# Performance work log

Hardware: AMD Instinct MI355X
Metric: run time of the kernel (lower is better)

The kernel has to match this reference:

```python
import jax, jax.numpy as jnp
import numpy as np

N, E = 50000, 800000
IN_C, HID, OUT_C = 100, 128, 40
LAYERS, GROUPS, CODES = 3, 3, 16
BETA = 0.98
EPS = 1e-5


def setup_inputs() -> dict:
    key = jax.random.key(0)
    ks = jax.random.split(key, 16)
    lin = lambda k, i, o: (jax.random.normal(k, (i, o), jnp.float32) / np.sqrt(i)).astype(jnp.float32)
    d = {}
    d["x"] = jax.random.normal(ks[0], (N, IN_C), jnp.float32)
    d["src"] = jax.random.randint(ks[1], (E,), 0, N, jnp.int32)
    d["dst"] = jax.random.randint(ks[2], (E,), 0, N, jnp.int32)
    # SAGEConv params: lin_l (aggregated, with bias) and lin_r (root, no bias)
    d["W0a"], d["W0r"], d["b0"] = lin(ks[3], IN_C, HID), lin(ks[4], IN_C, HID), jnp.zeros((HID,), jnp.float32)
    d["W1a"], d["W1r"], d["b1"] = lin(ks[5], HID, HID), lin(ks[6], HID, HID), jnp.zeros((HID,), jnp.float32)
    d["W2a"], d["W2r"], d["b2"] = lin(ks[7], HID, HID), lin(ks[8], HID, HID), jnp.zeros((HID,), jnp.float32)
    # BatchNorm (eval mode: running stats) for first num_layers-1 = 2 layers
    d["bn_gamma"] = jnp.ones((2, HID), jnp.float32)
    d["bn_beta"] = jnp.zeros((2, HID), jnp.float32)
    d["bn_mean"] = jnp.zeros((2, HID), jnp.float32)
    d["bn_var"] = jnp.ones((2, HID), jnp.float32)
    # Residual VQ codebooks: [layer, group, num_codes, feature]
    d["codebooks"] = 0.1 * jax.random.normal(ks[9], (LAYERS, GROUPS, CODES, HID), jnp.float32)
    d["lin_W"] = lin(ks[10], HID, OUT_C)
    d["lin_b"] = jnp.zeros((OUT_C,), jnp.float32)
    return d


def _sage_conv(h, src, dst, Wa, Wr, b):
    # mean neighbor aggregation (PyG SAGEConv, aggr='mean')
    msg = h[src]                                              # [E, d]
    agg = jax.ops.segment_sum(msg, dst, num_segments=N)       # [N, d]
    deg = jax.ops.segment_sum(jnp.ones((E,), h.dtype), dst, num_segments=N)
    agg = agg / jnp.maximum(deg, 1.0)[:, None]
    return agg @ Wa + b + h @ Wr


def _rvq(h, cb):
    # residual vector quantization over GROUPS codebooks; cb: [G, K, D]
    res, quant, ids = h, jnp.zeros_like(h), []
    for g in range(GROUPS):
        c = cb[g]                                             # [K, D]
        d2 = (jnp.sum(res * res, -1, keepdims=True)
              - 2.0 * res @ c.T + jnp.sum(c * c, -1))          # [N, K]
        idx = jnp.argmin(d2, axis=-1)
        q = c[idx]
        quant = quant + q
        res = res - q
        ids.append(idx)
    sg = jax.lax.stop_gradient
    loss = (BETA * jnp.mean((h - sg(quant)) ** 2)
            + (1.0 - BETA) * jnp.mean((sg(h) - quant) ** 2))
    return loss, jnp.stack(ids, axis=1)                        # [N, G] int


def reference(x, src, dst, W0a, W0r, b0, W1a, W1r, b1, W2a, W2r, b2,
              bn_gamma, bn_beta, bn_mean, bn_var, codebooks, lin_W, lin_b):
    Ws = [(W0a, W0r, b0), (W1a, W1r, b1), (W2a, W2r, b2)]
    h = x
    total_loss = jnp.float32(0.0)
    id_list = []
    for i in range(LAYERS - 1):
        h = _sage_conv(h, src, dst, *Ws[i])
        h = (h - bn_mean[i]) * jax.lax.rsqrt(bn_var[i] + EPS) * bn_gamma[i] + bn_beta[i]
        h = jax.nn.relu(h)                                     # dropout: eval mode (identity)
        loss, ids = _rvq(h, codebooks[i])
        total_loss = total_loss + loss
        id_list.append(ids)
    h = _sage_conv(h, src, dst, *Ws[-1])
    loss, ids = _rvq(h, codebooks[-1])
    total_loss = total_loss + loss
    id_list.append(ids)
    out = h @ lin_W + lin_b
    return out, total_loss, jnp.concatenate(id_list, axis=1)
```

## Files before the change

### kernel.cpp

```cpp
#include <hip/hip_runtime.h>

#define NN 50000
#define HID 128
#define IN_C 100
#define OUT_C 40

__global__ __launch_bounds__(256)
void hist_kernel(const int* __restrict__ dst, int* __restrict__ deg, int E) {
    int e = blockIdx.x * 256 + threadIdx.x;
    if (e < E) atomicAdd(&deg[dst[e]], 1);
}

__global__ __launch_bounds__(256)
void chunk_sum_kernel(const int* __restrict__ deg, int* __restrict__ chunk_sums, int N) {
    __shared__ int s[256];
    const int t = threadIdx.x;
    const int i = blockIdx.x * 256 + t;
    s[t] = (i < N) ? deg[i] : 0;
    __syncthreads();
    for (int o = 128; o; o >>= 1) { if (t < o) s[t] += s[t + o]; __syncthreads(); }
    if (t == 0) chunk_sums[blockIdx.x] = s[0];
}

__global__ __launch_bounds__(256)
void chunk_scan_kernel(int* __restrict__ chunk_sums, int M) {
    __shared__ int s[256];
    const int t = threadIdx.x;
    int v = (t < M) ? chunk_sums[t] : 0;
    s[t] = v;
    __syncthreads();
    for (int o = 1; o < 256; o <<= 1) {
        int x = (t >= o) ? s[t - o] : 0;
        __syncthreads();
        s[t] += x;
        __syncthreads();
    }
    if (t < M) chunk_sums[t] = s[t] - v;
}

__global__ __launch_bounds__(256)
void chunk_apply_kernel(const int* __restrict__ deg, const int* __restrict__ chunk_sums,
                        int* __restrict__ row_start, int* __restrict__ cursor, int N) {
    __shared__ int s[256];
    const int t = threadIdx.x;
    const int i = blockIdx.x * 256 + t;
    int v = (i < N) ? deg[i] : 0;
    s[t] = v;
    __syncthreads();
    for (int o = 1; o < 256; o <<= 1) {
        int x = (t >= o) ? s[t - o] : 0;
        __syncthreads();
        s[t] += x;
        __syncthreads();
    }
    if (i < N) {
        int ex = chunk_sums[blockIdx.x] + s[t] - v;
        row_start[i] = ex;
        cursor[i] = ex;
        if (i == N - 1) row_start[N] = ex + v;
    }
}

__global__ __launch_bounds__(256)
void scatter_kernel(const int* __restrict__ src, const int* __restrict__ dst,
                    int* __restrict__ cursor, int* __restrict__ csr_src, int E) {
    int e = blockIdx.x * 256 + threadIdx.x;
    if (e < E) {
        int pos = atomicAdd(&cursor[dst[e]], 1);
        csr_src[pos] = src[e];
    }
}

template<int K, bool HAS_BN, typename TIN>
__global__ __launch_bounds__(512, 6)
void layer_fused(const TIN* __restrict__ h_in,
                 const int* __restrict__ row_start, const int* __restrict__ csr_src,
                 const float* __restrict__ Wa, const float* __restrict__ Wr,
                 const float* __restrict__ b,
                 const float* __restrict__ gamma, const float* __restrict__ beta,
                 const float* __restrict__ mean, const float* __restrict__ var,
                 const float* __restrict__ cb,
                 double* __restrict__ h_out,
                 float* __restrict__ ids_out, int id_col0,
                 double* __restrict__ loss_part) {
    __shared__ double s_agg[8][HID];
    __shared__ double s_h[8][HID];
    __shared__ float s_cb[3 * 16 * 129];
    __shared__ float s_cc32[3][16];
    __shared__ double s_ws[8];
    const int t = threadIdx.x;
    const int w = t >> 6, lane = t & 63;
    const int n0 = blockIdx.x * 8;

    {
        const int n = n0 + w;
        const int r0 = row_start[n], r1 = row_start[n + 1];
        const int f0 = 2 * lane;
        if (f0 < K) {
            double a0 = 0.0, a1 = 0.0, c0 = 0.0, c1 = 0.0;
            int i = r0;
            for (; i + 1 < r1; i += 2) {
                const TIN* p0 = h_in + (size_t)csr_src[i] * K + f0;
                const TIN* p1 = h_in + (size_t)csr_src[i + 1] * K + f0;
                a0 += (double)p0[0]; a1 += (double)p0[1];
                c0 += (double)p1[0]; c1 += (double)p1[1];
            }
            if (i < r1) {
                const TIN* p0 = h_in + (size_t)csr_src[i] * K + f0;
                a0 += (double)p0[0]; a1 += (double)p0[1];
            }
            const int deg = r1 - r0;
            const double dd = (double)(deg > 1 ? deg : 1);
            const TIN* pr = h_in + (size_t)n * K + f0;
            s_agg[w][f0]     = (a0 + c0) / dd;
            s_agg[w][f0 + 1] = (a1 + c1) / dd;
            s_h[w][f0]     = (double)pr[0];
            s_h[w][f0 + 1] = (double)pr[1];
        }
    }
    __syncthreads();

    for (int idx = t; idx < 3 * 16 * 128; idx += 512)
        s_cb[(idx >> 7) * 129 + (idx & 127)] = cb[idx];

    const int col = t & 127;
    const int p4 = t >> 7;
    double accA = (double)b[col];
    double accB = accA;
#pragma unroll 4
    for (int k = 0; k < K; ++k) {
        const double wa = (double)Wa[(size_t)k * HID + col];
        const double wr = (double)Wr[(size_t)k * HID + col];
        accA += s_agg[p4][k] * wa + s_h[p4][k] * wr;
        accB += s_agg[p4 + 4][k] * wa + s_h[p4 + 4][k] * wr;
    }
    __syncthreads();

    {
        double scale = 1.0, shift = 0.0;
        if (HAS_BN) {
            scale = (double)gamma[col] / sqrt((double)var[col] + 1e-5);
            shift = (double)beta[col] - (double)mean[col] * scale;
        }
        double vA = accA, vB = accB;
        if (HAS_BN) {
            vA = vA * scale + shift; vA = vA > 0.0 ? vA : 0.0;
            vB = vB * scale + shift; vB = vB > 0.0 ? vB : 0.0;
        }
        h_out[(size_t)(n0 + p4) * HID + col] = vA;
        h_out[(size_t)(n0 + p4 + 4) * HID + col] = vB;
        s_agg[p4][col] = vA;
        s_agg[p4 + 4][col] = vB;
    }
    if (t < 48) {
        const float* c = &s_cb[t * 129];
        double s = 0.0;
        for (int j = 0; j < 128; j++) { double cj = (double)c[j]; s += cj * cj; }
        s_cc32[t >> 4][t & 15] = (float)s;
    }
    __syncthreads();

    {
        double* res = &s_agg[w][0];
        const int n = n0 + w;
        const int k = lane & 15, q = lane >> 4;

        for (int g = 0; g < 3; ++g) {
            double r0 = res[lane], r1 = res[lane + 64];
            double pr = r0 * r0 + r1 * r1;
            pr += __shfl_xor(pr, 1, 64);
            pr += __shfl_xor(pr, 2, 64);
            pr += __shfl_xor(pr, 4, 64);
            pr += __shfl_xor(pr, 8, 64);
            pr += __shfl_xor(pr, 16, 64);
            pr += __shfl_xor(pr, 32, 64);
            const float rr32 = (float)pr;

            const float* c = &s_cb[(g * 16 + k) * 129];
            double dot = 0.0;
#pragma unroll
            for (int j2 = 0; j2 < 32; ++j2) {
                int j = q * 32 + ((j2 + q * 8) & 31);
                dot += res[j] * (double)c[j];
            }
            dot += __shfl_xor(dot, 16, 64);
            dot += __shfl_xor(dot, 32, 64);

            const float rc32 = (float)dot;
            const float t1 = rr32 - 2.0f * rc32;
            const float d2 = t1 + s_cc32[g][k];

            float bv = d2; int bk = k;
            {
                float ov; int ok;
                ov = __shfl_xor(bv, 1, 64); ok = __shfl_xor(bk, 1, 64);
                if (ov < bv || (ov == bv && ok < bk)) { bv = ov; bk = ok; }
                ov = __shfl_xor(bv, 2, 64); ok = __shfl_xor(bk, 2, 64);
                if (ov < bv || (ov == bv && ok < bk)) { bv = ov; bk = ok; }
                ov = __shfl_xor(bv, 4, 64); ok = __shfl_xor(bk, 4, 64);
                if (ov < bv || (ov == bv && ok < bk)) { bv = ov; bk = ok; }
                ov = __shfl_xor(bv, 8, 64); ok = __shfl_xor(bk, 8, 64);
                if (ov < bv || (ov == bv && ok < bk)) { bv = ov; bk = ok; }
            }
            if (lane == 0)
                ids_out[(size_t)n * 9 + id_col0 + g] = (float)bk;

            res[lane]      -= (double)s_cb[(g * 16 + bk) * 129 + lane];
            res[lane + 64] -= (double)s_cb[(g * 16 + bk) * 129 + lane + 64];
        }
        double r0 = res[lane], r1 = res[lane + 64];
        double wl = r0 * r0 + r1 * r1;
        wl += __shfl_xor(wl, 1, 64);
        wl += __shfl_xor(wl, 2, 64);
        wl += __shfl_xor(wl, 4, 64);
        wl += __shfl_xor(wl, 8, 64);
        wl += __shfl_xor(wl, 16, 64);
        wl += __shfl_xor(wl, 32, 64);
        if (lane == 0) s_ws[w] = wl;
    }
    __syncthreads();
    if (t == 0) {
        double s = 0.0;
#pragma unroll
        for (int i = 0; i < 8; i++) s += s_ws[i];
        loss_part[blockIdx.x] = s;
    }
}

__global__ __launch_bounds__(128)
void linear_kernel(const double* __restrict__ h, const float* __restrict__ W,
                   const float* __restrict__ b, float* __restrict__ out, int N) {
    constexpr int NODES = 32;
    __shared__ float s_w[HID * OUT_C];
    __shared__ float s_b[OUT_C];
    __shared__ double s_h[HID];
    const int t = threadIdx.x;
    for (int idx = t; idx < HID * OUT_C; idx += 128) s_w[idx] = W[idx];
    if (t < OUT_C) s_b[t] = b[t];
    __syncthreads();
    const int n0 = blockIdx.x * NODES;
    for (int ni = 0; ni < NODES; ++ni) {
        int n = n0 + ni;
        if (n >= N) break;
        s_h[t] = h[(size_t)n * HID + t];
        __syncthreads();
        if (t < OUT_C) {
            double acc = (double)s_b[t];
            for (int kk = 0; kk < HID; kk++)
                acc += s_h[kk] * (double)s_w[kk * OUT_C + t];
            out[(size_t)n * OUT_C + t] = (float)acc;
        }
        __syncthreads();
    }
}

__global__ __launch_bounds__(256)
void finalize_kernel(const double* __restrict__ loss_part, int M,
                     float* __restrict__ out_loss) {
    __shared__ double s[256];
    const int t = threadIdx.x;
    double v = 0.0;
    for (int i = t; i < M; i += 256) v += loss_part[i];
    s[t] = v;
    __syncthreads();
    for (int off = 128; off; off >>= 1) {
        if (t < off) s[t] += s[t + off];
        __syncthreads();
    }
    if (t == 0) out_loss[0] = (float)(s[0] / ((double)NN * (double)HID));
}

extern "C" void kernel_launch(void* const* d_in, const int* in_sizes, int n_in,
                              void* d_out, int out_size, void* d_ws, size_t ws_size,
                              hipStream_t stream) {
    const float* x    = (const float*)d_in[0];
    const int*   src  = (const int*)d_in[1];
    const int*   dst  = (const int*)d_in[2];
    const float* W0a = (const float*)d_in[3];
    const float* W0r = (const float*)d_in[4];
    const float* b0  = (const float*)d_in[5];
    const float* W1a = (const float*)d_in[6];
    const float* W1r = (const float*)d_in[7];
    const float* b1  = (const float*)d_in[8];
    const float* W2a = (const float*)d_in[9];
    const float* W2r = (const float*)d_in[10];
    const float* b2  = (const float*)d_in[11];
    const float* bn_gamma = (const float*)d_in[12];
    const float* bn_beta  = (const float*)d_in[13];
    const float* bn_mean  = (const float*)d_in[14];
    const float* bn_var   = (const float*)d_in[15];
    const float* cb    = (const float*)d_in[16];
    const float* lin_W = (const float*)d_in[17];
    const float* lin_b = (const float*)d_in[18];

    const int E = in_sizes[1];

    float* out      = (float*)d_out;
    float* out_loss = out + (size_t)NN * OUT_C;
    float* out_ids  = out_loss + 1;

    char* base = (char*)d_ws;
    int* deg_i      = (int*)base;
    int* row_start  = deg_i + NN;
    int* cursor     = row_start + NN + 1;
    int* csr_src    = cursor + NN;
    int* chunk_sums = csr_src + E;
    size_t int_bytes = ((size_t)(3 * NN + 1 + E + 256) * 4 + 255) & ~(size_t)255;
    double* loss_part = (double*)(base + int_bytes);
    double* h1 = loss_part + 3 * 6250 + 6;
    double* h2 = h1 + (size_t)NN * HID;

    const int cb_layer = 3 * 16 * HID;
    const int NB = NN / 8;
    const int NCHUNK = (NN + 255) / 256;

    hipMemsetAsync(deg_i, 0, NN * sizeof(int), stream);
    hist_kernel<<<(E + 255) / 256, 256, 0, stream>>>(dst, deg_i, E);
    chunk_sum_kernel<<<NCHUNK, 256, 0, stream>>>(deg_i, chunk_sums, NN);
    chunk_scan_kernel<<<1, 256, 0, stream>>>(chunk_sums, NCHUNK);
    chunk_apply_kernel<<<NCHUNK, 256, 0, stream>>>(deg_i, chunk_sums, row_start, cursor, NN);
    scatter_kernel<<<(E + 255) / 256, 256, 0, stream>>>(src, dst, cursor, csr_src, E);

    layer_fused<IN_C, true, float><<<NB, 512, 0, stream>>>(
        x, row_start, csr_src, W0a, W0r, b0, bn_gamma, bn_beta, bn_mean, bn_var,
        cb + 0 * cb_layer, h1, out_ids, 0, loss_part);

    layer_fused<HID, true, double><<<NB, 512, 0, stream>>>(
        h1, row_start, csr_src, W1a, W1r, b1,
        bn_gamma + HID, bn_beta + HID, bn_mean + HID, bn_var + HID,
        cb + 1 * cb_layer, h2, out_ids, 3, loss_part + NB);

    layer_fused<HID, false, double><<<NB, 512, 0, stream>>>(
        h2, row_start, csr_src, W2a, W2r, b2, nullptr, nullptr, nullptr, nullptr,
        cb + 2 * cb_layer, h1, out_ids, 6, loss_part + 2 * NB);

    linear_kernel<<<(NN + 31) / 32, 128, 0, stream>>>(h1, lin_W, lin_b, out, NN);
    finalize_kernel<<<1, 256, 0, stream>>>(loss_part, 3 * NB, out_loss);
}
```

Measured before the change: 1.029 ms.

## Fold BatchNorm into pre-converted double2 weights and vectorize gather and GEMV

```diff
diff --git a/kernel.cpp b/kernel.cpp
--- a/kernel.cpp
+++ b/kernel.cpp
@@ -71,101 +71,128 @@
     }
 }
 
-template<int K, bool HAS_BN, typename TIN>
-__global__ __launch_bounds__(512, 6)
+__global__ __launch_bounds__(128)
+void prep_weights(const float* __restrict__ Wa, const float* __restrict__ Wr,
+                  const float* __restrict__ b,
+                  const float* __restrict__ gamma, const float* __restrict__ beta,
+                  const float* __restrict__ mean, const float* __restrict__ var,
+                  int has_bn,
+                  double2* __restrict__ Wa2, double2* __restrict__ Wr2,
+                  double* __restrict__ b64) {
+    const int col = threadIdx.x;
+    const int k2 = blockIdx.x;
+    double scale = 1.0, shift = 0.0;
+    if (has_bn) {
+        scale = (double)gamma[col] / sqrt((double)var[col] + 1e-5);
+        shift = (double)beta[col] - (double)mean[col] * scale;
+    }
+    double2 wa, wr;
+    wa.x = (double)Wa[(size_t)(2 * k2) * HID + col] * scale;
+    wa.y = (double)Wa[(size_t)(2 * k2 + 1) * HID + col] * scale;
+    wr.x = (double)Wr[(size_t)(2 * k2) * HID + col] * scale;
+    wr.y = (double)Wr[(size_t)(2 * k2 + 1) * HID + col] * scale;
+    Wa2[(size_t)k2 * HID + col] = wa;
+    Wr2[(size_t)k2 * HID + col] = wr;
+    if (k2 == 0) b64[col] = (double)b[col] * scale + shift;
+}
+
+__device__ __forceinline__ double2 ld2(const double* p) {
+    return *(const double2*)p;
+}
+__device__ __forceinline__ double2 ld2(const float* p) {
+    float2 v = *(const float2*)p;
+    return make_double2((double)v.x, (double)v.y);
+}
+
+template<int K, bool RELU, typename TIN>
+__global__ __launch_bounds__(512, 8)
 void layer_fused(const TIN* __restrict__ h_in,
                  const int* __restrict__ row_start, const int* __restrict__ csr_src,
-                 const float* __restrict__ Wa, const float* __restrict__ Wr,
-                 const float* __restrict__ b,
-                 const float* __restrict__ gamma, const float* __restrict__ beta,
-                 const float* __restrict__ mean, const float* __restrict__ var,
+                 const double2* __restrict__ Wa2, const double2* __restrict__ Wr2,
+                 const double* __restrict__ b64,
                  const float* __restrict__ cb,
                  double* __restrict__ h_out,
                  float* __restrict__ ids_out, int id_col0,
                  double* __restrict__ loss_part) {
     __shared__ double s_agg[8][HID];
     __shared__ double s_h[8][HID];
-    __shared__ float s_cb[3 * 16 * 129];
-    __shared__ float s_cc32[3][16];
-    __shared__ double s_ws[8];
+    __shared__ float s_cb[3 * 16 * HID];
     const int t = threadIdx.x;
     const int w = t >> 6, lane = t & 63;
     const int n0 = blockIdx.x * 8;
+
+    for (int idx = t; idx < 3 * 16 * HID; idx += 512) s_cb[idx] = cb[idx];
 
     {
         const int n = n0 + w;
         const int r0 = row_start[n], r1 = row_start[n + 1];
         const int f0 = 2 * lane;
         if (f0 < K) {
-            double a0 = 0.0, a1 = 0.0, c0 = 0.0, c1 = 0.0;
+            double s0 = 0, s1 = 0, s2 = 0, s3 = 0, s4 = 0, s5 = 0, s6 = 0, s7 = 0;
             int i = r0;
-            for (; i + 1 < r1; i += 2) {
-                const TIN* p0 = h_in + (size_t)csr_src[i] * K + f0;
-                const TIN* p1 = h_in + (size_t)csr_src[i + 1] * K + f0;
-                a0 += (double)p0[0]; a1 += (double)p0[1];
-                c0 += (double)p1[0]; c1 += (double)p1[1];
+            for (; i + 3 < r1; i += 4) {
+                double2 v0 = ld2(h_in + (size_t)csr_src[i] * K + f0);
+                double2 v1 = ld2(h_in + (size_t)csr_src[i + 1] * K + f0);
+                double2 v2 = ld2(h_in + (size_t)csr_src[i + 2] * K + f0);
+                double2 v3 = ld2(h_in + (size_t)csr_src[i + 3] * K + f0);
+                s0 += v0.x; s1 += v0.y; s2 += v1.x; s3 += v1.y;
+                s4 += v2.x; s5 += v2.y; s6 += v3.x; s7 += v3.y;
             }
-            if (i < r1) {
-                const TIN* p0 = h_in + (size_t)csr_src[i] * K + f0;
-                a0 += (double)p0[0]; a1 += (double)p0[1];
+            for (; i < r1; ++i) {
+                double2 v = ld2(h_in + (size_t)csr_src[i] * K + f0);
+                s0 += v.x; s1 += v.y;
             }
             const int deg = r1 - r0;
             const double dd = (double)(deg > 1 ? deg : 1);
-            const TIN* pr = h_in + (size_t)n * K + f0;
-            s_agg[w][f0]     = (a0 + c0) / dd;
-            s_agg[w][f0 + 1] = (a1 + c1) / dd;
-            s_h[w][f0]     = (double)pr[0];
-            s_h[w][f0 + 1] = (double)pr[1];
+            const double2 root = ld2(h_in + (size_t)n * K + f0);
+            s_agg[w][f0]     = ((s0 + s2) + (s4 + s6)) / dd;
+            s_agg[w][f0 + 1] = ((s1 + s3) + (s5 + s7)) / dd;
+            s_h[w][f0]     = root.x;
+            s_h[w][f0 + 1] = root.y;
         }
     }
     __syncthreads();
-
-    for (int idx = t; idx < 3 * 16 * 128; idx += 512)
-        s_cb[(idx >> 7) * 129 + (idx & 127)] = cb[idx];
 
     const int col = t & 127;
     const int p4 = t >> 7;
-    double accA = (double)b[col];
+    double accA = b64[col];
     double accB = accA;
-#pragma unroll 4
-    for (int k = 0; k < K; ++k) {
-        const double wa = (double)Wa[(size_t)k * HID + col];
-        const double wr = (double)Wr[(size_t)k * HID + col];
-        accA += s_agg[p4][k] * wa + s_h[p4][k] * wr;
-        accB += s_agg[p4 + 4][k] * wa + s_h[p4 + 4][k] * wr;
+#pragma unroll 2
+    for (int k2 = 0; k2 < K / 2; ++k2) {
+        const double2 WA = Wa2[(size_t)k2 * HID + col];
+        const double2 WR = Wr2[(size_t)k2 * HID + col];
+        const double2 gA = *(const double2*)&s_agg[p4][2 * k2];
+        const double2 hA = *(const double2*)&s_h[p4][2 * k2];
+        const double2 gB = *(const double2*)&s_agg[p4 + 4][2 * k2];
+        const double2 hB = *(const double2*)&s_h[p4 + 4][2 * k2];
+        accA += gA.x * WA.x + hA.x * WR.x + gA.y * WA.y + hA.y * WR.y;
+        accB += gB.x * WA.x + hB.x * WR.x + gB.y * WA.y + hB.y * WR.y;
     }
     __syncthreads();
 
     {
-        double scale = 1.0, shift = 0.0;
-        if (HAS_BN) {
-            scale = (double)gamma[col] / sqrt((double)var[col] + 1e-5);
-            shift = (double)beta[col] - (double)mean[col] * scale;
-        }
         double vA = accA, vB = accB;
-        if (HAS_BN) {
-            vA = vA * scale + shift; vA = vA > 0.0 ? vA : 0.0;
-            vB = vB * scale + shift; vB = vB > 0.0 ? vB : 0.0;
+        if (RELU) {
+            vA = vA > 0.0 ? vA : 0.0;
+            vB = vB > 0.0 ? vB : 0.0;
         }
         h_out[(size_t)(n0 + p4) * HID + col] = vA;
         h_out[(size_t)(n0 + p4 + 4) * HID + col] = vB;
         s_agg[p4][col] = vA;
         s_agg[p4 + 4][col] = vB;
     }
-    if (t < 48) {
-        const float* c = &s_cb[t * 129];
-        double s = 0.0;
-        for (int j = 0; j < 128; j++) { double cj = (double)c[j]; s += cj * cj; }
-        s_cc32[t >> 4][t & 15] = (float)s;
-    }
     __syncthreads();
 
     {
         double* res = &s_agg[w][0];
+        double* s_ws = &s_h[0][0];
         const int n = n0 + w;
         const int k = lane & 15, q = lane >> 4;
+        const int jbase = q * 32;
+        const int rot = (k + 8 * q) & 31;
 
         for (int g = 0; g < 3; ++g) {
+            const float* c = &s_cb[(g * 16 + k) * HID];
             double r0 = res[lane], r1 = res[lane + 64];
             double pr = r0 * r0 + r1 * r1;
             pr += __shfl_xor(pr, 1, 64);
@@ -176,19 +203,23 @@
             pr += __shfl_xor(pr, 32, 64);
             const float rr32 = (float)pr;
 
-            const float* c = &s_cb[(g * 16 + k) * 129];
-            double dot = 0.0;
+            double cc = 0.0, dot = 0.0;
 #pragma unroll
             for (int j2 = 0; j2 < 32; ++j2) {
-                int j = q * 32 + ((j2 + q * 8) & 31);
-                dot += res[j] * (double)c[j];
+                const int j = jbase + ((j2 + rot) & 31);
+                const double cj = (double)c[j];
+                cc += cj * cj;
+                dot += res[j] * cj;
             }
+            cc += __shfl_xor(cc, 16, 64);
+            cc += __shfl_xor(cc, 32, 64);
             dot += __shfl_xor(dot, 16, 64);
             dot += __shfl_xor(dot, 32, 64);
 
+            const float cc32 = (float)cc;
             const float rc32 = (float)dot;
             const float t1 = rr32 - 2.0f * rc32;
-            const float d2 = t1 + s_cc32[g][k];
+            const float d2 = t1 + cc32;
 
             float bv = d2; int bk = k;
             {
@@ -205,8 +236,9 @@
             if (lane == 0)
                 ids_out[(size_t)n * 9 + id_col0 + g] = (float)bk;
 
-            res[lane]      -= (double)s_cb[(g * 16 + bk) * 129 + lane];
-            res[lane + 64] -= (double)s_cb[(g * 16 + bk) * 129 + lane + 64];
+            const float* cbest = &s_cb[(g * 16 + bk) * HID];
+            res[lane]      -= (double)cbest[lane];
+            res[lane + 64] -= (double)cbest[lane + 64];
         }
         double r0 = res[lane], r1 = res[lane + 64];
         double wl = r0 * r0 + r1 * r1;
@@ -220,6 +252,7 @@
     }
     __syncthreads();
     if (t == 0) {
+        const double* s_ws = &s_h[0][0];
         double s = 0.0;
 #pragma unroll
         for (int i = 0; i < 8; i++) s += s_ws[i];
@@ -309,6 +342,15 @@
     double* loss_part = (double*)(base + int_bytes);
     double* h1 = loss_part + 3 * 6250 + 6;
     double* h2 = h1 + (size_t)NN * HID;
+    double2* w0a2 = (double2*)(h2 + (size_t)NN * HID);
+    double2* w0r2 = w0a2 + 50 * HID;
+    double2* w1a2 = w0r2 + 50 * HID;
+    double2* w1r2 = w1a2 + 64 * HID;
+    double2* w2a2 = w1r2 + 64 * HID;
+    double2* w2r2 = w2a2 + 64 * HID;
+    double* b0_64 = (double*)(w2r2 + 64 * HID);
+    double* b1_64 = b0_64 + HID;
+    double* b2_64 = b1_64 + HID;
 
     const int cb_layer = 3 * 16 * HID;
     const int NB = NN / 8;
@@ -321,17 +363,23 @@
     chunk_apply_kernel<<<NCHUNK, 256, 0, stream>>>(deg_i, chunk_sums, row_start, cursor, NN);
     scatter_kernel<<<(E + 255) / 256, 256, 0, stream>>>(src, dst, cursor, csr_src, E);
 
+    prep_weights<<<IN_C / 2, 128, 0, stream>>>(W0a, W0r, b0, bn_gamma, bn_beta,
+                                               bn_mean, bn_var, 1, w0a2, w0r2, b0_64);
+    prep_weights<<<HID / 2, 128, 0, stream>>>(W1a, W1r, b1, bn_gamma + HID, bn_beta + HID,
+                                              bn_mean + HID, bn_var + HID, 1, w1a2, w1r2, b1_64);
+    prep_weights<<<HID / 2, 128, 0, stream>>>(W2a, W2r, b2, nullptr, nullptr,
+                                              nullptr, nullptr, 0, w2a2, w2r2, b2_64);
+
     layer_fused<IN_C, true, float><<<NB, 512, 0, stream>>>(
-        x, row_start, csr_src, W0a, W0r, b0, bn_gamma, bn_beta, bn_mean, bn_var,
+        x, row_start, csr_src, w0a2, w0r2, b0_64,
         cb + 0 * cb_layer, h1, out_ids, 0, loss_part);
 
     layer_fused<HID, true, double><<<NB, 512, 0, stream>>>(
-        h1, row_start, csr_src, W1a, W1r, b1,
-        bn_gamma + HID, bn_beta + HID, bn_mean + HID, bn_var + HID,
+        h1, row_start, csr_src, w1a2, w1r2, b1_64,
         cb + 1 * cb_layer, h2, out_ids, 3, loss_part + NB);
 
     layer_fused<HID, false, double><<<NB, 512, 0, stream>>>(
-        h2, row_start, csr_src, W2a, W2r, b2, nullptr, nullptr, nullptr, nullptr,
+        h2, row_start, csr_src, w2a2, w2r2, b2_64,
         cb + 2 * cb_layer, h1, out_ids, 6, loss_part + 2 * NB);
 
     linear_kernel<<<(NN + 31) / 32, 128, 0, stream>>>(h1, lin_W, lin_b, out, NN);
```

Result: slower. 1.476 ms (+43.4%).

## Store hidden activations as float, pack weights, vectorize gathers, inline codebook norms

Applied to the files above, without the earlier changes.

```diff
diff --git a/kernel.cpp b/kernel.cpp
--- a/kernel.cpp
+++ b/kernel.cpp
@@ -71,57 +71,67 @@
     }
 }
 
-template<int K, bool HAS_BN, typename TIN>
-__global__ __launch_bounds__(512, 6)
-void layer_fused(const TIN* __restrict__ h_in,
+__global__ __launch_bounds__(128)
+void prep_pack(const float* __restrict__ Wa, const float* __restrict__ Wr,
+               float2* __restrict__ wp) {
+    const int k = blockIdx.x, col = threadIdx.x;
+    float2 v;
+    v.x = Wa[(size_t)k * HID + col];
+    v.y = Wr[(size_t)k * HID + col];
+    wp[(size_t)k * HID + col] = v;
+}
+
+template<int K, bool HAS_BN>
+__global__ __launch_bounds__(512, 8)
+void layer_fused(const float* __restrict__ h_in,
                  const int* __restrict__ row_start, const int* __restrict__ csr_src,
-                 const float* __restrict__ Wa, const float* __restrict__ Wr,
-                 const float* __restrict__ b,
+                 const float2* __restrict__ wp, const float* __restrict__ b,
                  const float* __restrict__ gamma, const float* __restrict__ beta,
                  const float* __restrict__ mean, const float* __restrict__ var,
                  const float* __restrict__ cb,
-                 double* __restrict__ h_out,
+                 float* __restrict__ h_out,
                  float* __restrict__ ids_out, int id_col0,
                  double* __restrict__ loss_part) {
     __shared__ double s_agg[8][HID];
     __shared__ double s_h[8][HID];
-    __shared__ float s_cb[3 * 16 * 129];
-    __shared__ float s_cc32[3][16];
-    __shared__ double s_ws[8];
+    __shared__ float s_cb[3 * 16 * HID];
     const int t = threadIdx.x;
     const int w = t >> 6, lane = t & 63;
     const int n0 = blockIdx.x * 8;
+
+    for (int idx = t; idx < 3 * 16 * HID; idx += 512) s_cb[idx] = cb[idx];
 
     {
         const int n = n0 + w;
         const int r0 = row_start[n], r1 = row_start[n + 1];
         const int f0 = 2 * lane;
         if (f0 < K) {
-            double a0 = 0.0, a1 = 0.0, c0 = 0.0, c1 = 0.0;
+            double s0 = 0, s1 = 0, s2 = 0, s3 = 0, s4 = 0, s5 = 0, s6 = 0, s7 = 0;
             int i = r0;
-            for (; i + 1 < r1; i += 2) {
-                const TIN* p0 = h_in + (size_t)csr_src[i] * K + f0;
-                const TIN* p1 = h_in + (size_t)csr_src[i + 1] * K + f0;
-                a0 += (double)p0[0]; a1 += (double)p0[1];
-                c0 += (double)p1[0]; c1 += (double)p1[1];
+            for (; i + 3 < r1; i += 4) {
+                float2 v0 = *(const float2*)(h_in + (size_t)csr_src[i] * K + f0);
+                float2 v1 = *(const float2*)(h_in + (size_t)csr_src[i + 1] * K + f0);
+                float2 v2 = *(const float2*)(h_in + (size_t)csr_src[i + 2] * K + f0);
+                float2 v3 = *(const float2*)(h_in + (size_t)csr_src[i + 3] * K + f0);
+                s0 += (double)v0.x; s1 += (double)v0.y;
+                s2 += (double)v1.x; s3 += (double)v1.y;
+                s4 += (double)v2.x; s5 += (double)v2.y;
+                s6 += (double)v3.x; s7 += (double)v3.y;
             }
-            if (i < r1) {
-                const TIN* p0 = h_in + (size_t)csr_src[i] * K + f0;
-                a0 += (double)p0[0]; a1 += (double)p0[1];
+            for (; i < r1; ++i) {
+                float2 v = *(const float2*)(h_in + (size_t)csr_src[i] * K + f0);
+                s0 += (double)v.x; s1 += (double)v.y;
             }
             const int deg = r1 - r0;
             const double dd = (double)(deg > 1 ? deg : 1);
-            const TIN* pr = h_in + (size_t)n * K + f0;
-            s_agg[w][f0]     = (a0 + c0) / dd;
-            s_agg[w][f0 + 1] = (a1 + c1) / dd;
-            s_h[w][f0]     = (double)pr[0];
-            s_h[w][f0 + 1] = (double)pr[1];
+            float2 root = *(const float2*)(h_in + (size_t)n * K + f0);
+            s_agg[w][f0]     = ((s0 + s2) + (s4 + s6)) / dd;
+            s_agg[w][f0 + 1] = ((s1 + s3) + (s5 + s7)) / dd;
+            s_h[w][f0]     = (double)root.x;
+            s_h[w][f0 + 1] = (double)root.y;
         }
     }
     __syncthreads();
-
-    for (int idx = t; idx < 3 * 16 * 128; idx += 512)
-        s_cb[(idx >> 7) * 129 + (idx & 127)] = cb[idx];
 
     const int col = t & 127;
     const int p4 = t >> 7;
@@ -129,43 +139,39 @@
     double accB = accA;
 #pragma unroll 4
     for (int k = 0; k < K; ++k) {
-        const double wa = (double)Wa[(size_t)k * HID + col];
-        const double wr = (double)Wr[(size_t)k * HID + col];
+        const float2 wv = wp[(size_t)k * HID + col];
+        const double wa = (double)wv.x, wr = (double)wv.y;
         accA += s_agg[p4][k] * wa + s_h[p4][k] * wr;
         accB += s_agg[p4 + 4][k] * wa + s_h[p4 + 4][k] * wr;
     }
     __syncthreads();
 
     {
-        double scale = 1.0, shift = 0.0;
-        if (HAS_BN) {
-            scale = (double)gamma[col] / sqrt((double)var[col] + 1e-5);
-            shift = (double)beta[col] - (double)mean[col] * scale;
-        }
         double vA = accA, vB = accB;
         if (HAS_BN) {
+            const double scale = (double)gamma[col] / sqrt((double)var[col] + 1e-5);
+            const double shift = (double)beta[col] - (double)mean[col] * scale;
             vA = vA * scale + shift; vA = vA > 0.0 ? vA : 0.0;
             vB = vB * scale + shift; vB = vB > 0.0 ? vB : 0.0;
         }
-        h_out[(size_t)(n0 + p4) * HID + col] = vA;
-        h_out[(size_t)(n0 + p4 + 4) * HID + col] = vB;
-        s_agg[p4][col] = vA;
-        s_agg[p4 + 4][col] = vB;
-    }
-    if (t < 48) {
-        const float* c = &s_cb[t * 129];
-        double s = 0.0;
-        for (int j = 0; j < 128; j++) { double cj = (double)c[j]; s += cj * cj; }
-        s_cc32[t >> 4][t & 15] = (float)s;
+        const float fA = (float)vA, fB = (float)vB;
+        h_out[(size_t)(n0 + p4) * HID + col] = fA;
+        h_out[(size_t)(n0 + p4 + 4) * HID + col] = fB;
+        s_agg[p4][col] = (double)fA;
+        s_agg[p4 + 4][col] = (double)fB;
     }
     __syncthreads();
 
     {
         double* res = &s_agg[w][0];
+        double* s_ws = &s_h[0][0];
         const int n = n0 + w;
         const int k = lane & 15, q = lane >> 4;
+        const int jbase = q * 32;
+        const int rot = (k + 8 * q) & 31;
 
         for (int g = 0; g < 3; ++g) {
+            const float* c = &s_cb[(g * 16 + k) * HID];
             double r0 = res[lane], r1 = res[lane + 64];
             double pr = r0 * r0 + r1 * r1;
             pr += __shfl_xor(pr, 1, 64);
@@ -176,19 +182,23 @@
             pr += __shfl_xor(pr, 32, 64);
             const float rr32 = (float)pr;
 
-            const float* c = &s_cb[(g * 16 + k) * 129];
-            double dot = 0.0;
+            double cc = 0.0, dot = 0.0;
 #pragma unroll
             for (int j2 = 0; j2 < 32; ++j2) {
-                int j = q * 32 + ((j2 + q * 8) & 31);
-                dot += res[j] * (double)c[j];
+                const int j = jbase + ((j2 + rot) & 31);
+                const double cj = (double)c[j];
+                cc += cj * cj;
+                dot += res[j] * cj;
             }
+            cc += __shfl_xor(cc, 16, 64);
+            cc += __shfl_xor(cc, 32, 64);
             dot += __shfl_xor(dot, 16, 64);
             dot += __shfl_xor(dot, 32, 64);
 
+            const float cc32 = (float)cc;
             const float rc32 = (float)dot;
             const float t1 = rr32 - 2.0f * rc32;
-            const float d2 = t1 + s_cc32[g][k];
+            const float d2 = t1 + cc32;
 
             float bv = d2; int bk = k;
             {
@@ -205,8 +215,9 @@
             if (lane == 0)
                 ids_out[(size_t)n * 9 + id_col0 + g] = (float)bk;
 
-            res[lane]      -= (double)s_cb[(g * 16 + bk) * 129 + lane];
-            res[lane + 64] -= (double)s_cb[(g * 16 + bk) * 129 + lane + 64];
+            const float* cbest = &s_cb[(g * 16 + bk) * HID];
+            res[lane]      -= (double)cbest[lane];
+            res[lane + 64] -= (double)cbest[lane + 64];
         }
         double r0 = res[lane], r1 = res[lane + 64];
         double wl = r0 * r0 + r1 * r1;
@@ -220,6 +231,7 @@
     }
     __syncthreads();
     if (t == 0) {
+        const double* s_ws = &s_h[0][0];
         double s = 0.0;
 #pragma unroll
         for (int i = 0; i < 8; i++) s += s_ws[i];
@@ -228,12 +240,12 @@
 }
 
 __global__ __launch_bounds__(128)
-void linear_kernel(const double* __restrict__ h, const float* __restrict__ W,
+void linear_kernel(const float* __restrict__ h, const float* __restrict__ W,
                    const float* __restrict__ b, float* __restrict__ out, int N) {
     constexpr int NODES = 32;
     __shared__ float s_w[HID * OUT_C];
     __shared__ float s_b[OUT_C];
-    __shared__ double s_h[HID];
+    __shared__ float s_h[HID];
     const int t = threadIdx.x;
     for (int idx = t; idx < HID * OUT_C; idx += 128) s_w[idx] = W[idx];
     if (t < OUT_C) s_b[t] = b[t];
@@ -247,7 +259,7 @@
         if (t < OUT_C) {
             double acc = (double)s_b[t];
             for (int kk = 0; kk < HID; kk++)
-                acc += s_h[kk] * (double)s_w[kk * OUT_C + t];
+                acc += (double)s_h[kk] * (double)s_w[kk * OUT_C + t];
             out[(size_t)n * OUT_C + t] = (float)acc;
         }
         __syncthreads();
@@ -307,8 +319,11 @@
     int* chunk_sums = csr_src + E;
     size_t int_bytes = ((size_t)(3 * NN + 1 + E + 256) * 4 + 255) & ~(size_t)255;
     double* loss_part = (double*)(base + int_bytes);
-    double* h1 = loss_part + 3 * 6250 + 6;
-    double* h2 = h1 + (size_t)NN * HID;
+    float* h1 = (float*)(loss_part + 3 * 6250);
+    float* h2 = h1 + (size_t)NN * HID;
+    float2* wp0 = (float2*)(h2 + (size_t)NN * HID);
+    float2* wp1 = wp0 + (size_t)IN_C * HID;
+    float2* wp2 = wp1 + (size_t)HID * HID;
 
     const int cb_layer = 3 * 16 * HID;
     const int NB = NN / 8;
@@ -321,17 +336,21 @@
     chunk_apply_kernel<<<NCHUNK, 256, 0, stream>>>(deg_i, chunk_sums, row_start, cursor, NN);
     scatter_kernel<<<(E + 255) / 256, 256, 0, stream>>>(src, dst, cursor, csr_src, E);
 
-    layer_fused<IN_C, true, float><<<NB, 512, 0, stream>>>(
-        x, row_start, csr_src, W0a, W0r, b0, bn_gamma, bn_beta, bn_mean, bn_var,
+    prep_pack<<<IN_C, 128, 0, stream>>>(W0a, W0r, wp0);
+    prep_pack<<<HID, 128, 0, stream>>>(W1a, W1r, wp1);
+    prep_pack<<<HID, 128, 0, stream>>>(W2a, W2r, wp2);
+
+    layer_fused<IN_C, true><<<NB, 512, 0, stream>>>(
+        x, row_start, csr_src, wp0, b0, bn_gamma, bn_beta, bn_mean, bn_var,
         cb + 0 * cb_layer, h1, out_ids, 0, loss_part);
 
-    layer_fused<HID, true, double><<<NB, 512, 0, stream>>>(
-        h1, row_start, csr_src, W1a, W1r, b1,
+    layer_fused<HID, true><<<NB, 512, 0, stream>>>(
+        h1, row_start, csr_src, wp1, b1,
         bn_gamma + HID, bn_beta + HID, bn_mean + HID, bn_var + HID,
         cb + 1 * cb_layer, h2, out_ids, 3, loss_part + NB);
 
-    layer_fused<HID, false, double><<<NB, 512, 0, stream>>>(
-        h2, row_start, csr_src, W2a, W2r, b2, nullptr, nullptr, nullptr, nullptr,
+    layer_fused<HID, false><<<NB, 512, 0, stream>>>(
+        h2, row_start, csr_src, wp2, b2, nullptr, nullptr, nullptr, nullptr,
         cb + 2 * cb_layer, h1, out_ids, 6, loss_part + 2 * NB);
 
     linear_kernel<<<(NN + 31) / 32, 128, 0, stream>>>(h1, lin_W, lin_b, out, NN);
```

Measured after the change: 1.262 ms. 22.6% more time.
